# Kernel optimization log

Hardware: AMD Instinct MI355X
Metric: run time of the kernel (lower is better)

## Reference

```python
import jax, jax.numpy as jnp
import numpy as np

E = 64          # num_experts
DIM = 1024      # model dim
HID = 512       # per-expert FFN hidden dim
N = 65536       # total routed tokens (1024 per expert)


def setup_inputs() -> dict:
    key = jax.random.key(0)
    k_x, k1, k2, k3 = jax.random.split(key, 4)
    x = jax.random.normal(k_x, (N, DIM), dtype=jnp.float32)
    # learned params: w1/w3 [E, HID, DIM], w2 [E, DIM, HID] (trunc_normal std 0.02 ~ normal*0.02)
    w1 = jax.random.normal(k1, (E, HID, DIM), dtype=jnp.float32) * 0.02
    w2 = jax.random.normal(k2, (E, DIM, HID), dtype=jnp.float32) * 0.02
    w3 = jax.random.normal(k3, (E, HID, DIM), dtype=jnp.float32) * 0.02
    num_tokens_per_expert = jnp.full((E,), N // E, dtype=jnp.int32)
    return {"x": x, "w1": w1, "w2": w2, "w3": w3,
            "num_tokens_per_expert": num_tokens_per_expert}


def reference(x, w1, w2, w3, num_tokens_per_expert):
    # Grouped-GEMM SwiGLU expert FFN (torch._grouped_mm path, bf16 compute).
    bf16 = jnp.bfloat16
    xb = x.astype(bf16)                                   # [N, DIM]
    g = num_tokens_per_expert                             # [E] int32 group sizes
    w1t = jnp.swapaxes(w1.astype(bf16), 1, 2)             # [E, DIM, HID]
    w3t = jnp.swapaxes(w3.astype(bf16), 1, 2)             # [E, DIM, HID]
    w2t = jnp.swapaxes(w2.astype(bf16), 1, 2)             # [E, HID, DIM]
    h = jax.nn.silu(jax.lax.ragged_dot(xb, w1t, g))       # [N, HID]
    h = h * jax.lax.ragged_dot(xb, w3t, g)                # fused gate
    out = jax.lax.ragged_dot(h, w2t, g)                   # [N, DIM]
    return out.astype(x.dtype)
```

## Files before the change

### kernel.cpp

```cpp
#include <hip/hip_runtime.h>
#include <hip/hip_bf16.h>
#include <stdint.h>

#define NE   64
#define DIM  1024
#define HID  512
#define TPE  1024

typedef __attribute__((ext_vector_type(8)))  __bf16          bf16x8;
typedef __attribute__((ext_vector_type(16))) float           f32x16;
typedef __attribute__((ext_vector_type(8)))  unsigned short  ushort8_t;
typedef __attribute__((ext_vector_type(4)))  unsigned short  ushort4_t;
typedef __attribute__((ext_vector_type(4)))  float           float4_t;

__device__ __forceinline__ unsigned short f2bf(float f) {
  return __builtin_bit_cast(unsigned short, static_cast<__bf16>(f));
}
__device__ __forceinline__ float bf2f(unsigned short u) {
  unsigned int x = ((unsigned int)u) << 16;
  return __builtin_bit_cast(float, x);
}
__device__ __forceinline__ ushort4_t pack4(float4_t v) {
  ushort4_t r;
  r[0] = f2bf(v[0]); r[1] = f2bf(v[1]); r[2] = f2bf(v[2]); r[3] = f2bf(v[3]);
  return r;
}

#define LDK 40

#define P1_NKT (DIM / 32)

__global__ __launch_bounds__(256, 2) void p1_kernel(
    const float* __restrict__ X, const float* __restrict__ W1,
    const float* __restrict__ W3, unsigned short* __restrict__ H) {
  __shared__ __align__(16) unsigned short lA [2][128 * LDK];
  __shared__ __align__(16) unsigned short lB1[2][128 * LDK];
  __shared__ __align__(16) unsigned short lB3[2][128 * LDK];

  const int bid = blockIdx.x;
  const int e   = bid >> 5;
  const int tm  = (bid >> 2) & 7;
  const int tn  = bid & 3;
  const int t   = threadIdx.x;

  const float* gA  = X  + (size_t)(e * TPE + tm * 128) * DIM;
  const float* gB1 = W1 + ((size_t)e * HID + tn * 128) * DIM;
  const float* gB3 = W3 + ((size_t)e * HID + tn * 128) * DIM;

  float4_t ra[4], rb1[4], rb3[4];

  auto load_tile = [&](int kt) {
#pragma unroll
    for (int i = 0; i < 4; ++i) {
      const int f = t + 256 * i;
      const int row = f >> 3, c4 = f & 7;
      const size_t off = (size_t)row * DIM + kt * 32 + c4 * 4;
      ra [i] = *reinterpret_cast<const float4_t*>(gA  + off);
      rb1[i] = *reinterpret_cast<const float4_t*>(gB1 + off);
      rb3[i] = *reinterpret_cast<const float4_t*>(gB3 + off);
    }
  };
  auto store_tile = [&](int buf) {
#pragma unroll
    for (int i = 0; i < 4; ++i) {
      const int f = t + 256 * i;
      const int row = f >> 3, c4 = f & 7;
      const int idx = row * LDK + c4 * 4;
      *reinterpret_cast<ushort4_t*>(&lA [buf][idx]) = pack4(ra [i]);
      *reinterpret_cast<ushort4_t*>(&lB1[buf][idx]) = pack4(rb1[i]);
      *reinterpret_cast<ushort4_t*>(&lB3[buf][idx]) = pack4(rb3[i]);
    }
  };

  const int lane = t & 63;
  const int wv   = t >> 6;
  const int wr   = wv >> 1, wc = wv & 1;
  const int lr   = lane & 31;
  const int ks   = lane >> 5;

  const int aoff0 = (wr * 64 + lr) * LDK + ks * 8;
  const int boff0 = (wc * 64 + lr) * LDK + ks * 8;

  f32x16 acc1[2][2], acc3[2][2];
#pragma unroll
  for (int m = 0; m < 2; ++m)
#pragma unroll
    for (int n = 0; n < 2; ++n)
#pragma unroll
      for (int i = 0; i < 16; ++i) { acc1[m][n][i] = 0.f; acc3[m][n][i] = 0.f; }

  load_tile(0);
  for (int kt = 0; kt < P1_NKT; ++kt) {
    const int buf = kt & 1;
    store_tile(buf);
    __syncthreads();
    if (kt + 1 < P1_NKT) load_tile(kt + 1);
#pragma unroll
    for (int kk = 0; kk < 2; ++kk) {
      bf16x8 a[2], b1[2], b3[2];
#pragma unroll
      for (int m = 0; m < 2; ++m)
        a[m] = __builtin_bit_cast(bf16x8, *reinterpret_cast<const ushort8_t*>(
                   &lA[buf][aoff0 + m * (32 * LDK) + kk * 16]));
#pragma unroll
      for (int n = 0; n < 2; ++n) {
        b1[n] = __builtin_bit_cast(bf16x8, *reinterpret_cast<const ushort8_t*>(
                    &lB1[buf][boff0 + n * (32 * LDK) + kk * 16]));
        b3[n] = __builtin_bit_cast(bf16x8, *reinterpret_cast<const ushort8_t*>(
                    &lB3[buf][boff0 + n * (32 * LDK) + kk * 16]));
      }
#pragma unroll
      for (int m = 0; m < 2; ++m)
#pragma unroll
        for (int n = 0; n < 2; ++n) {
          acc1[m][n] = __builtin_amdgcn_mfma_f32_32x32x16_bf16(a[m], b1[n], acc1[m][n], 0, 0, 0);
          acc3[m][n] = __builtin_amdgcn_mfma_f32_32x32x16_bf16(a[m], b3[n], acc3[m][n], 0, 0, 0);
        }
    }
  }

  const int tokBase = e * TPE + tm * 128 + wr * 64;
  const int hidBase = tn * 128 + wc * 64;
#pragma unroll
  for (int m = 0; m < 2; ++m)
#pragma unroll
    for (int n = 0; n < 2; ++n)
#pragma unroll
      for (int r = 0; r < 16; ++r) {
        const int rr  = (r & 3) + 8 * (r >> 2) + 4 * ks;
        const int tok = tokBase + m * 32 + rr;
        const int hid = hidBase + n * 32 + lr;
        const float av = bf2f(f2bf(acc1[m][n][r]));
        const float bv = bf2f(f2bf(acc3[m][n][r]));
        const float s  = av / (1.0f + __expf(-av));
        H[(size_t)tok * HID + hid] = f2bf(s * bv);
      }
}

#define P2_NKT (HID / 32)

__global__ __launch_bounds__(256, 2) void p2_kernel(
    const unsigned short* __restrict__ Hin, const float* __restrict__ W2,
    float* __restrict__ OUT) {
  __shared__ __align__(16) unsigned short lA[2][128 * LDK];
  __shared__ __align__(16) unsigned short lB[2][128 * LDK];

  const int bid = blockIdx.x;
  const int e   = bid >> 6;
  const int tm  = (bid >> 3) & 7;
  const int tn  = bid & 7;
  const int t   = threadIdx.x;

  const unsigned short* gA = Hin + (size_t)(e * TPE + tm * 128) * HID;
  const float*          gB = W2  + ((size_t)e * DIM + tn * 128) * HID;

  ushort8_t ra[2];
  float4_t  rb[4];

  auto load_tile = [&](int kt) {
#pragma unroll
    for (int i = 0; i < 2; ++i) {
      const int f = t + 256 * i;
      const int row = f >> 2, c8 = f & 3;
      ra[i] = *reinterpret_cast<const ushort8_t*>(gA + (size_t)row * HID + kt * 32 + c8 * 8);
    }
#pragma unroll
    for (int i = 0; i < 4; ++i) {
      const int f = t + 256 * i;
      const int row = f >> 3, c4 = f & 7;
      rb[i] = *reinterpret_cast<const float4_t*>(gB + (size_t)row * HID + kt * 32 + c4 * 4);
    }
  };
  auto store_tile = [&](int buf) {
#pragma unroll
    for (int i = 0; i < 2; ++i) {
      const int f = t + 256 * i;
      const int row = f >> 2, c8 = f & 3;
      *reinterpret_cast<ushort8_t*>(&lA[buf][row * LDK + c8 * 8]) = ra[i];
    }
#pragma unroll
    for (int i = 0; i < 4; ++i) {
      const int f = t + 256 * i;
      const int row = f >> 3, c4 = f & 7;
      *reinterpret_cast<ushort4_t*>(&lB[buf][row * LDK + c4 * 4]) = pack4(rb[i]);
    }
  };

  const int lane = t & 63;
  const int wv   = t >> 6;
  const int wr   = wv >> 1, wc = wv & 1;
  const int lr   = lane & 31;
  const int ks   = lane >> 5;

  const int aoff0 = (wr * 64 + lr) * LDK + ks * 8;
  const int boff0 = (wc * 64 + lr) * LDK + ks * 8;

  f32x16 acc[2][2];
#pragma unroll
  for (int m = 0; m < 2; ++m)
#pragma unroll
    for (int n = 0; n < 2; ++n)
#pragma unroll
      for (int i = 0; i < 16; ++i) acc[m][n][i] = 0.f;

  load_tile(0);
  for (int kt = 0; kt < P2_NKT; ++kt) {
    const int buf = kt & 1;
    store_tile(buf);
    __syncthreads();
    if (kt + 1 < P2_NKT) load_tile(kt + 1);
#pragma unroll
    for (int kk = 0; kk < 2; ++kk) {
      bf16x8 a[2], b[2];
#pragma unroll
      for (int m = 0; m < 2; ++m)
        a[m] = __builtin_bit_cast(bf16x8, *reinterpret_cast<const ushort8_t*>(
                   &lA[buf][aoff0 + m * (32 * LDK) + kk * 16]));
#pragma unroll
      for (int n = 0; n < 2; ++n)
        b[n] = __builtin_bit_cast(bf16x8, *reinterpret_cast<const ushort8_t*>(
                   &lB[buf][boff0 + n * (32 * LDK) + kk * 16]));
#pragma unroll
      for (int m = 0; m < 2; ++m)
#pragma unroll
        for (int n = 0; n < 2; ++n)
          acc[m][n] = __builtin_amdgcn_mfma_f32_32x32x16_bf16(a[m], b[n], acc[m][n], 0, 0, 0);
    }
  }

  const int tokBase = e * TPE + tm * 128 + wr * 64;
  const int dBase   = tn * 128 + wc * 64;
#pragma unroll
  for (int m = 0; m < 2; ++m)
#pragma unroll
    for (int n = 0; n < 2; ++n)
#pragma unroll
      for (int r = 0; r < 16; ++r) {
        const int rr  = (r & 3) + 8 * (r >> 2) + 4 * ks;
        const int tok = tokBase + m * 32 + rr;
        const int d   = dBase + n * 32 + lr;
        OUT[(size_t)tok * DIM + d] = bf2f(f2bf(acc[m][n][r]));
      }
}

extern "C" void kernel_launch(void* const* d_in, const int* in_sizes, int n_in,
                              void* d_out, int out_size, void* d_ws, size_t ws_size,
                              hipStream_t stream) {
  (void)in_sizes; (void)n_in; (void)out_size; (void)ws_size;
  const float* X  = (const float*)d_in[0];
  const float* W1 = (const float*)d_in[1];
  const float* W2 = (const float*)d_in[2];
  const float* W3 = (const float*)d_in[3];

  unsigned short* H = (unsigned short*)d_ws;
  float* OUT = (float*)d_out;

  p1_kernel<<<dim3(NE * 8 * 4), dim3(256), 0, stream>>>(X, W1, W3, H);
  p2_kernel<<<dim3(NE * 8 * 8), dim3(256), 0, stream>>>(H, W2, OUT);
}
```

Measured before the change: 444.3 us.

## Shrink P1 N-tile, raise occupancy, swizzle blocks across XCDs, widen LDS stores

P1's per-block hidden tile shrinks from 128 to 64 columns, which halves its accumulators and B-tile LDS and doubles the grid to 4096 blocks. Both kernels now ask for 4 blocks per CU in their launch bounds. A block-ID swizzle keeps the tiles of one expert on the same XCD so its weights are reused in L2. Global loads and LDS stores are regrouped into 8-element bf16 writes. The aim is more parallelism and fewer register/LDS limits, at the cost of reloading X twice as often in P1 and possible register spills under the tighter bounds.

```diff
diff --git a/kernel.cpp b/kernel.cpp
--- a/kernel.cpp
+++ b/kernel.cpp
@@ -10,7 +10,6 @@
 typedef __attribute__((ext_vector_type(8)))  __bf16          bf16x8;
 typedef __attribute__((ext_vector_type(16))) float           f32x16;
 typedef __attribute__((ext_vector_type(8)))  unsigned short  ushort8_t;
-typedef __attribute__((ext_vector_type(4)))  unsigned short  ushort4_t;
 typedef __attribute__((ext_vector_type(4)))  float           float4_t;
 
 __device__ __forceinline__ unsigned short f2bf(float f) {
@@ -20,56 +19,63 @@
   unsigned int x = ((unsigned int)u) << 16;
   return __builtin_bit_cast(float, x);
 }
-__device__ __forceinline__ ushort4_t pack4(float4_t v) {
-  ushort4_t r;
-  r[0] = f2bf(v[0]); r[1] = f2bf(v[1]); r[2] = f2bf(v[2]); r[3] = f2bf(v[3]);
+__device__ __forceinline__ ushort8_t pack8(float4_t a, float4_t b) {
+  ushort8_t r;
+  r[0] = f2bf(a[0]); r[1] = f2bf(a[1]); r[2] = f2bf(a[2]); r[3] = f2bf(a[3]);
+  r[4] = f2bf(b[0]); r[5] = f2bf(b[1]); r[6] = f2bf(b[2]); r[7] = f2bf(b[3]);
   return r;
 }
 
 #define LDK 40
 
+__device__ __forceinline__ int xcd_swizzle(int bid, int nwg) {
+  return (bid & 7) * (nwg >> 3) + (bid >> 3);
+}
+
 #define P1_NKT (DIM / 32)
 
-__global__ __launch_bounds__(256, 2) void p1_kernel(
+__global__ __launch_bounds__(256, 4) void p1_kernel(
     const float* __restrict__ X, const float* __restrict__ W1,
     const float* __restrict__ W3, unsigned short* __restrict__ H) {
   __shared__ __align__(16) unsigned short lA [2][128 * LDK];
-  __shared__ __align__(16) unsigned short lB1[2][128 * LDK];
-  __shared__ __align__(16) unsigned short lB3[2][128 * LDK];
-
-  const int bid = blockIdx.x;
-  const int e   = bid >> 5;
-  const int tm  = (bid >> 2) & 7;
-  const int tn  = bid & 3;
-  const int t   = threadIdx.x;
+  __shared__ __align__(16) unsigned short lB1[2][ 64 * LDK];
+  __shared__ __align__(16) unsigned short lB3[2][ 64 * LDK];
+
+  const int tile = xcd_swizzle(blockIdx.x, NE * 8 * 8);
+  const int e  = tile >> 6;
+  const int tm = (tile >> 3) & 7;
+  const int tn = tile & 7;
+  const int t  = threadIdx.x;
 
   const float* gA  = X  + (size_t)(e * TPE + tm * 128) * DIM;
-  const float* gB1 = W1 + ((size_t)e * HID + tn * 128) * DIM;
-  const float* gB3 = W3 + ((size_t)e * HID + tn * 128) * DIM;
-
-  float4_t ra[4], rb1[4], rb3[4];
+  const float* gB1 = W1 + ((size_t)e * HID + tn * 64) * DIM;
+  const float* gB3 = W3 + ((size_t)e * HID + tn * 64) * DIM;
+
+  float4_t ra[2][2], rb1[2], rb3[2];
+
+  const int arow0 = t >> 2, acol = (t & 3) * 8;
+  const int brow  = t >> 2, bcol = (t & 3) * 8;
 
   auto load_tile = [&](int kt) {
 #pragma unroll
-    for (int i = 0; i < 4; ++i) {
-      const int f = t + 256 * i;
-      const int row = f >> 3, c4 = f & 7;
-      const size_t off = (size_t)row * DIM + kt * 32 + c4 * 4;
-      ra [i] = *reinterpret_cast<const float4_t*>(gA  + off);
-      rb1[i] = *reinterpret_cast<const float4_t*>(gB1 + off);
-      rb3[i] = *reinterpret_cast<const float4_t*>(gB3 + off);
-    }
+    for (int i = 0; i < 2; ++i) {
+      const size_t off = (size_t)(arow0 + 64 * i) * DIM + kt * 32 + acol;
+      ra[i][0] = *reinterpret_cast<const float4_t*>(gA + off);
+      ra[i][1] = *reinterpret_cast<const float4_t*>(gA + off + 4);
+    }
+    const size_t boff = (size_t)brow * DIM + kt * 32 + bcol;
+    rb1[0] = *reinterpret_cast<const float4_t*>(gB1 + boff);
+    rb1[1] = *reinterpret_cast<const float4_t*>(gB1 + boff + 4);
+    rb3[0] = *reinterpret_cast<const float4_t*>(gB3 + boff);
+    rb3[1] = *reinterpret_cast<const float4_t*>(gB3 + boff + 4);
   };
   auto store_tile = [&](int buf) {
 #pragma unroll
-    for (int i = 0; i < 4; ++i) {
-      const int f = t + 256 * i;
-      const int row = f >> 3, c4 = f & 7;
-      const int idx = row * LDK + c4 * 4;
-      *reinterpret_cast<ushort4_t*>(&lA [buf][idx]) = pack4(ra [i]);
-      *reinterpret_cast<ushort4_t*>(&lB1[buf][idx]) = pack4(rb1[i]);
-      *reinterpret_cast<ushort4_t*>(&lB3[buf][idx]) = pack4(rb3[i]);
-    }
+    for (int i = 0; i < 2; ++i)
+      *reinterpret_cast<ushort8_t*>(&lA[buf][(arow0 + 64 * i) * LDK + acol]) =
+          pack8(ra[i][0], ra[i][1]);
+    *reinterpret_cast<ushort8_t*>(&lB1[buf][brow * LDK + bcol]) = pack8(rb1[0], rb1[1]);
+    *reinterpret_cast<ushort8_t*>(&lB3[buf][brow * LDK + bcol]) = pack8(rb3[0], rb3[1]);
   };
 
   const int lane = t & 63;
@@ -79,15 +85,13 @@
   const int ks   = lane >> 5;
 
   const int aoff0 = (wr * 64 + lr) * LDK + ks * 8;
-  const int boff0 = (wc * 64 + lr) * LDK + ks * 8;
-
-  f32x16 acc1[2][2], acc3[2][2];
-#pragma unroll
-  for (int m = 0; m < 2; ++m)
-#pragma unroll
-    for (int n = 0; n < 2; ++n)
-#pragma unroll
-      for (int i = 0; i < 16; ++i) { acc1[m][n][i] = 0.f; acc3[m][n][i] = 0.f; }
+  const int boff0 = (wc * 32 + lr) * LDK + ks * 8;
+
+  f32x16 acc1[2], acc3[2];
+#pragma unroll
+  for (int m = 0; m < 2; ++m)
+#pragma unroll
+    for (int i = 0; i < 16; ++i) { acc1[m][i] = 0.f; acc3[m][i] = 0.f; }
 
   load_tile(0);
   for (int kt = 0; kt < P1_NKT; ++kt) {
@@ -97,92 +101,76 @@
     if (kt + 1 < P1_NKT) load_tile(kt + 1);
 #pragma unroll
     for (int kk = 0; kk < 2; ++kk) {
-      bf16x8 a[2], b1[2], b3[2];
+      bf16x8 a[2], b1, b3;
 #pragma unroll
       for (int m = 0; m < 2; ++m)
         a[m] = __builtin_bit_cast(bf16x8, *reinterpret_cast<const ushort8_t*>(
                    &lA[buf][aoff0 + m * (32 * LDK) + kk * 16]));
-#pragma unroll
-      for (int n = 0; n < 2; ++n) {
-        b1[n] = __builtin_bit_cast(bf16x8, *reinterpret_cast<const ushort8_t*>(
-                    &lB1[buf][boff0 + n * (32 * LDK) + kk * 16]));
-        b3[n] = __builtin_bit_cast(bf16x8, *reinterpret_cast<const ushort8_t*>(
-                    &lB3[buf][boff0 + n * (32 * LDK) + kk * 16]));
+      b1 = __builtin_bit_cast(bf16x8, *reinterpret_cast<const ushort8_t*>(
+               &lB1[buf][boff0 + kk * 16]));
+      b3 = __builtin_bit_cast(bf16x8, *reinterpret_cast<const ushort8_t*>(
+               &lB3[buf][boff0 + kk * 16]));
+#pragma unroll
+      for (int m = 0; m < 2; ++m) {
+        acc1[m] = __builtin_amdgcn_mfma_f32_32x32x16_bf16(a[m], b1, acc1[m], 0, 0, 0);
+        acc3[m] = __builtin_amdgcn_mfma_f32_32x32x16_bf16(a[m], b3, acc3[m], 0, 0, 0);
       }
-#pragma unroll
-      for (int m = 0; m < 2; ++m)
-#pragma unroll
-        for (int n = 0; n < 2; ++n) {
-          acc1[m][n] = __builtin_amdgcn_mfma_f32_32x32x16_bf16(a[m], b1[n], acc1[m][n], 0, 0, 0);
-          acc3[m][n] = __builtin_amdgcn_mfma_f32_32x32x16_bf16(a[m], b3[n], acc3[m][n], 0, 0, 0);
-        }
     }
   }
 
   const int tokBase = e * TPE + tm * 128 + wr * 64;
-  const int hidBase = tn * 128 + wc * 64;
-#pragma unroll
-  for (int m = 0; m < 2; ++m)
-#pragma unroll
-    for (int n = 0; n < 2; ++n)
-#pragma unroll
-      for (int r = 0; r < 16; ++r) {
-        const int rr  = (r & 3) + 8 * (r >> 2) + 4 * ks;
-        const int tok = tokBase + m * 32 + rr;
-        const int hid = hidBase + n * 32 + lr;
-        const float av = bf2f(f2bf(acc1[m][n][r]));
-        const float bv = bf2f(f2bf(acc3[m][n][r]));
-        const float s  = av / (1.0f + __expf(-av));
-        H[(size_t)tok * HID + hid] = f2bf(s * bv);
-      }
+  const int hid     = tn * 64 + wc * 32 + lr;
+#pragma unroll
+  for (int m = 0; m < 2; ++m)
+#pragma unroll
+    for (int r = 0; r < 16; ++r) {
+      const int rr  = (r & 3) + 8 * (r >> 2) + 4 * ks;
+      const int tok = tokBase + m * 32 + rr;
+      const float av = bf2f(f2bf(acc1[m][r]));
+      const float bv = bf2f(f2bf(acc3[m][r]));
+      const float s  = av / (1.0f + __expf(-av));
+      H[(size_t)tok * HID + hid] = f2bf(s * bv);
+    }
 }
 
 #define P2_NKT (HID / 32)
 
-__global__ __launch_bounds__(256, 2) void p2_kernel(
+__global__ __launch_bounds__(256, 4) void p2_kernel(
     const unsigned short* __restrict__ Hin, const float* __restrict__ W2,
     float* __restrict__ OUT) {
   __shared__ __align__(16) unsigned short lA[2][128 * LDK];
   __shared__ __align__(16) unsigned short lB[2][128 * LDK];
 
-  const int bid = blockIdx.x;
-  const int e   = bid >> 6;
-  const int tm  = (bid >> 3) & 7;
-  const int tn  = bid & 7;
-  const int t   = threadIdx.x;
+  const int tile = xcd_swizzle(blockIdx.x, NE * 8 * 8);
+  const int e  = tile >> 6;
+  const int tm = (tile >> 3) & 7;
+  const int tn = tile & 7;
+  const int t  = threadIdx.x;
 
   const unsigned short* gA = Hin + (size_t)(e * TPE + tm * 128) * HID;
   const float*          gB = W2  + ((size_t)e * DIM + tn * 128) * HID;
 
   ushort8_t ra[2];
-  float4_t  rb[4];
+  float4_t  rb[2][2];
+
+  const int row0 = t >> 2, col = (t & 3) * 8;
 
   auto load_tile = [&](int kt) {
 #pragma unroll
     for (int i = 0; i < 2; ++i) {
-      const int f = t + 256 * i;
-      const int row = f >> 2, c8 = f & 3;
-      ra[i] = *reinterpret_cast<const ushort8_t*>(gA + (size_t)row * HID + kt * 32 + c8 * 8);
-    }
-#pragma unroll
-    for (int i = 0; i < 4; ++i) {
-      const int f = t + 256 * i;
-      const int row = f >> 3, c4 = f & 7;
-      rb[i] = *reinterpret_cast<const float4_t*>(gB + (size_t)row * HID + kt * 32 + c4 * 4);
+      ra[i] = *reinterpret_cast<const ushort8_t*>(
+          gA + (size_t)(row0 + 64 * i) * HID + kt * 32 + col);
+      const size_t off = (size_t)(row0 + 64 * i) * HID + kt * 32 + col;
+      rb[i][0] = *reinterpret_cast<const float4_t*>(gB + off);
+      rb[i][1] = *reinterpret_cast<const float4_t*>(gB + off + 4);
     }
   };
   auto store_tile = [&](int buf) {
 #pragma unroll
     for (int i = 0; i < 2; ++i) {
-      const int f = t + 256 * i;
-      const int row = f >> 2, c8 = f & 3;
-      *reinterpret_cast<ushort8_t*>(&lA[buf][row * LDK + c8 * 8]) = ra[i];
-    }
-#pragma unroll
-    for (int i = 0; i < 4; ++i) {
-      const int f = t + 256 * i;
-      const int row = f >> 3, c4 = f & 7;
-      *reinterpret_cast<ushort4_t*>(&lB[buf][row * LDK + c4 * 4]) = pack4(rb[i]);
+      const int idx = (row0 + 64 * i) * LDK + col;
+      *reinterpret_cast<ushort8_t*>(&lA[buf][idx]) = ra[i];
+      *reinterpret_cast<ushort8_t*>(&lB[buf][idx]) = pack8(rb[i][0], rb[i][1]);
     }
   };
 
@@ -255,6 +243,6 @@
   unsigned short* H = (unsigned short*)d_ws;
   float* OUT = (float*)d_out;
 
-  p1_kernel<<<dim3(NE * 8 * 4), dim3(256), 0, stream>>>(X, W1, W3, H);
+  p1_kernel<<<dim3(NE * 8 * 8), dim3(256), 0, stream>>>(X, W1, W3, H);
   p2_kernel<<<dim3(NE * 8 * 8), dim3(256), 0, stream>>>(H, W2, OUT);
 }
```

After: 424.7 us. 4.4% less time.
